# Kernel optimization log

Measured on AMD Instinct MI355X. Metric: run time of the kernel, lower is better.

The kernel has to match this reference:

```python
import jax, jax.numpy as jnp
import numpy as np

E, H, I, T = 8, 1024, 2816, 8192  # experts, hidden, intermediate, total tokens


def setup_inputs() -> dict:
    key = jax.random.key(0)
    k1, k2, k3, k4 = jax.random.split(key, 4)
    x = jax.random.normal(k1, (T, H), dtype=jnp.float32)
    # xavier_normal std = sqrt(2 / (fan_in + fan_out))
    std = (2.0 / (H + I)) ** 0.5
    gate = jax.random.normal(k2, (E, H, I), dtype=jnp.float32) * std
    up = jax.random.normal(k3, (E, H, I), dtype=jnp.float32) * std
    down = jax.random.normal(k4, (E, I, H), dtype=jnp.float32) * std
    # tokens are pre-permuted so each expert's tokens are contiguous; equal split here
    tokens_per_expert = jnp.full((E,), T // E, dtype=jnp.int32)
    return {
        "permuted_local_hidden_states": x,
        "grouped_gate_proj": gate,
        "grouped_up_proj": up,
        "grouped_down_proj": down,
        "tokens_per_expert": tokens_per_expert,
    }


def reference(permuted_local_hidden_states, grouped_gate_proj, grouped_up_proj,
              grouped_down_proj, tokens_per_expert):
    # grouped GEMM: for expert e, rows in its contiguous segment are multiplied by W[e]
    o1 = jax.lax.ragged_dot(permuted_local_hidden_states, grouped_gate_proj,
                            tokens_per_expert)            # [T, I]
    o2 = jax.lax.ragged_dot(permuted_local_hidden_states, grouped_up_proj,
                            tokens_per_expert)            # [T, I]
    inter = jax.nn.silu(o1) * o2                          # SwiGLU  [T, I]
    out = jax.lax.ragged_dot(inter, grouped_down_proj, tokens_per_expert)  # [T, H]
    return out
```

## Files before the change

kernel.cpp:

```cpp
#include <hip/hip_runtime.h>
#include <hip/hip_bf16.h>


#define E_ 8
#define H_ 1024
#define I_ 2816
#define T_ 8192

typedef unsigned short u16;
typedef __attribute__((ext_vector_type(8))) short s16x8;
typedef __attribute__((ext_vector_type(8))) unsigned short u16x8;
typedef __attribute__((ext_vector_type(4))) float f32x4;

__device__ __forceinline__ void async16(const u16* g, u16* l) {
  __builtin_amdgcn_global_load_lds((__attribute__((address_space(1))) void*)g,
                                   (__attribute__((address_space(3))) void*)l, 16, 0, 0);
}

__device__ __forceinline__ u16 f2b(float f) {
  union { __hip_bfloat16 h; u16 u; } c;
  c.h = __float2bfloat16(f);
  return c.u;
}

__global__ __launch_bounds__(256) void convx_k(const float* __restrict__ x,
                                               u16* __restrict__ xb) {
  size_t i = ((size_t)blockIdx.x * 256 + threadIdx.x) * 8;
  float4 v0 = *(const float4*)(x + i);
  float4 v1 = *(const float4*)(x + i + 4);
  u16x8 b;
  b[0] = f2b(v0.x); b[1] = f2b(v0.y); b[2] = f2b(v0.z); b[3] = f2b(v0.w);
  b[4] = f2b(v1.x); b[5] = f2b(v1.y); b[6] = f2b(v1.z); b[7] = f2b(v1.w);
  *(u16x8*)(xb + i) = b;
}

template <int R, int C>
__device__ __forceinline__ void tconv_tile(const float* __restrict__ in,
                                           u16* __restrict__ out,
                                           int bx, int by, int t) {
  const int c0 = bx * 64, r0 = by * 64;
  const int c = c0 + (t >> 2);
  const int rq = (t & 3) * 8;
  const float* p = in + (size_t)r0 * C + c;
  u16* o = out + (size_t)c * R + r0;
  u16x8 b;
#pragma unroll
  for (int j = 0; j < 8; ++j) b[j] = f2b(p[(size_t)(rq + j) * C]);
  *(u16x8*)(o + rq) = b;
#pragma unroll
  for (int j = 0; j < 8; ++j) b[j] = f2b(p[(size_t)(32 + rq + j) * C]);
  *(u16x8*)(o + 32 + rq) = b;
}

__global__ __launch_bounds__(256) void tconvGU_k(const float* __restrict__ G,
                                                 const float* __restrict__ U,
                                                 u16* __restrict__ GT,
                                                 u16* __restrict__ UT) {
  const int z = blockIdx.z;
  const size_t eoff = (size_t)(z >> 1) * (size_t)H_ * I_;
  const float* in = ((z & 1) ? U : G) + eoff;
  u16* out = ((z & 1) ? UT : GT) + eoff;
  tconv_tile<H_, I_>(in, out, blockIdx.x, blockIdx.y, threadIdx.x);
}

__global__ __launch_bounds__(256) void tconvD_k(const float* __restrict__ D,
                                                u16* __restrict__ DT) {
  const size_t eoff = (size_t)blockIdx.z * (size_t)H_ * I_;
  tconv_tile<I_, H_>(D + eoff, DT + eoff, blockIdx.x, blockIdx.y, threadIdx.x);
}

__global__ __launch_bounds__(256, 2) void gemm12_k(
    const u16* __restrict__ X, const u16* __restrict__ GT,
    const u16* __restrict__ UT, const int* __restrict__ tpe,
    u16* __restrict__ inter) {
  __shared__ u16 sA[128 * 64];
  __shared__ u16 sG[64 * 64];
  __shared__ u16 sU[64 * 64];
  const int t = threadIdx.x;
  const int m0 = blockIdx.y * 128;
  const int n0 = blockIdx.x * 64;

  int e = 0, seg_end = T_;
  {
    int s = 0;
    for (int i = 0; i < E_; ++i) {
      int c = tpe[i];
      if (m0 < s + c) { e = i; seg_end = s + c; break; }
      s += c;
    }
  }
  const u16* GTe = GT + (size_t)e * I_ * H_;
  const u16* UTe = UT + (size_t)e * I_ * H_;

  const int sj = ((t & 7) ^ ((t >> 3) & 7)) * 8;
  const u16* gA = X + (size_t)(m0 + (t >> 3)) * H_ + sj;
  const u16* gG = GTe + (size_t)(n0 + (t >> 3)) * H_ + sj;
  const u16* gU = UTe + (size_t)(n0 + (t >> 3)) * H_ + sj;
  u16* lA = sA + t * 8;
  u16* lG = sG + t * 8;
  u16* lU = sU + t * 8;

  const int l = t & 63, w = t >> 6;
  const int wm = (w & 1) * 64, wn = (w >> 1) * 32;
  const int c0 = (((l >> 4) ^ (l & 7))) * 8;
  const u16* fA = sA + (size_t)(wm + (l & 15)) * 64;
  const u16* fG = sG + (size_t)(wn + (l & 15)) * 64;
  const u16* fU = sU + (size_t)(wn + (l & 15)) * 64;

  f32x4 accG[4][2], accU[4][2];
#pragma unroll
  for (int mi = 0; mi < 4; ++mi)
#pragma unroll
    for (int ni = 0; ni < 2; ++ni) {
      accG[mi][ni] = (f32x4){0.f, 0.f, 0.f, 0.f};
      accU[mi][ni] = (f32x4){0.f, 0.f, 0.f, 0.f};
    }

  for (int k0 = 0; k0 < H_; k0 += 64) {
    async16(gA + k0, lA);
    async16(gA + 32 * H_ + k0, lA + 2048);
    async16(gA + 64 * H_ + k0, lA + 4096);
    async16(gA + 96 * H_ + k0, lA + 6144);
    async16(gG + k0, lG);
    async16(gG + 32 * H_ + k0, lG + 2048);
    async16(gU + k0, lU);
    async16(gU + 32 * H_ + k0, lU + 2048);
    __syncthreads();
#pragma unroll
    for (int ks = 0; ks < 2; ++ks) {
      const int co = c0 ^ (ks * 32);
      s16x8 aF[4], gF[2], uF[2];
#pragma unroll
      for (int mi = 0; mi < 4; ++mi) aF[mi] = *(const s16x8*)(fA + mi * 1024 + co);
#pragma unroll
      for (int ni = 0; ni < 2; ++ni) {
        gF[ni] = *(const s16x8*)(fG + ni * 1024 + co);
        uF[ni] = *(const s16x8*)(fU + ni * 1024 + co);
      }
#pragma unroll
      for (int mi = 0; mi < 4; ++mi)
#pragma unroll
        for (int ni = 0; ni < 2; ++ni) {
          accG[mi][ni] = __builtin_amdgcn_mfma_f32_16x16x32_bf16(aF[mi], gF[ni], accG[mi][ni], 0, 0, 0);
          accU[mi][ni] = __builtin_amdgcn_mfma_f32_16x16x32_bf16(aF[mi], uF[ni], accU[mi][ni], 0, 0, 0);
        }
    }
    __syncthreads();
  }

  const int colb = l & 15, rowb = (l >> 4) * 4;
#pragma unroll
  for (int mi = 0; mi < 4; ++mi)
#pragma unroll
    for (int ni = 0; ni < 2; ++ni) {
      const size_t gcol = (size_t)(n0 + wn + ni * 16 + colb);
#pragma unroll
      for (int r = 0; r < 4; ++r) {
        int grow = m0 + wm + mi * 16 + rowb + r;
        if (grow < seg_end) {
          float o1 = accG[mi][ni][r];
          float o2 = accU[mi][ni][r];
          float sv = o1 / (1.f + __expf(-o1));
          inter[(size_t)grow * I_ + gcol] = f2b(sv * o2);
        }
      }
    }
}

__global__ __launch_bounds__(256, 2) void gemm3_k(
    const u16* __restrict__ A, const u16* __restrict__ DT,
    const int* __restrict__ tpe, float* __restrict__ out) {
  __shared__ u16 sA[128 * 64];
  __shared__ u16 sB[64 * 64];
  const int t = threadIdx.x;
  const int m0 = blockIdx.y * 128;
  const int n0 = blockIdx.x * 64;

  int e = 0, seg_end = T_;
  {
    int s = 0;
    for (int i = 0; i < E_; ++i) {
      int c = tpe[i];
      if (m0 < s + c) { e = i; seg_end = s + c; break; }
      s += c;
    }
  }
  const u16* DTe = DT + (size_t)e * H_ * I_;

  const int sj = ((t & 7) ^ ((t >> 3) & 7)) * 8;
  const u16* gA = A + (size_t)(m0 + (t >> 3)) * I_ + sj;
  const u16* gB = DTe + (size_t)(n0 + (t >> 3)) * I_ + sj;
  u16* lA = sA + t * 8;
  u16* lB = sB + t * 8;

  const int l = t & 63, w = t >> 6;
  const int wm = (w & 1) * 64, wn = (w >> 1) * 32;
  const int c0 = (((l >> 4) ^ (l & 7))) * 8;
  const u16* fA = sA + (size_t)(wm + (l & 15)) * 64;
  const u16* fB = sB + (size_t)(wn + (l & 15)) * 64;

  f32x4 acc[4][2];
#pragma unroll
  for (int mi = 0; mi < 4; ++mi)
#pragma unroll
    for (int ni = 0; ni < 2; ++ni) acc[mi][ni] = (f32x4){0.f, 0.f, 0.f, 0.f};

  for (int k0 = 0; k0 < I_; k0 += 64) {
    async16(gA + k0, lA);
    async16(gA + 32 * I_ + k0, lA + 2048);
    async16(gA + 64 * I_ + k0, lA + 4096);
    async16(gA + 96 * I_ + k0, lA + 6144);
    async16(gB + k0, lB);
    async16(gB + 32 * I_ + k0, lB + 2048);
    __syncthreads();
#pragma unroll
    for (int ks = 0; ks < 2; ++ks) {
      const int co = c0 ^ (ks * 32);
      s16x8 aF[4], bF[2];
#pragma unroll
      for (int mi = 0; mi < 4; ++mi) aF[mi] = *(const s16x8*)(fA + mi * 1024 + co);
#pragma unroll
      for (int ni = 0; ni < 2; ++ni) bF[ni] = *(const s16x8*)(fB + ni * 1024 + co);
#pragma unroll
      for (int mi = 0; mi < 4; ++mi)
#pragma unroll
        for (int ni = 0; ni < 2; ++ni)
          acc[mi][ni] = __builtin_amdgcn_mfma_f32_16x16x32_bf16(aF[mi], bF[ni], acc[mi][ni], 0, 0, 0);
    }
    __syncthreads();
  }

  const int colb = l & 15, rowb = (l >> 4) * 4;
#pragma unroll
  for (int mi = 0; mi < 4; ++mi)
#pragma unroll
    for (int ni = 0; ni < 2; ++ni) {
      const size_t gcol = (size_t)(n0 + wn + ni * 16 + colb);
#pragma unroll
      for (int r = 0; r < 4; ++r) {
        int grow = m0 + wm + mi * 16 + rowb + r;
        if (grow < seg_end) out[(size_t)grow * H_ + gcol] = acc[mi][ni][r];
      }
    }
}

extern "C" void kernel_launch(void* const* d_in, const int* in_sizes, int n_in,
                              void* d_out, int out_size, void* d_ws, size_t ws_size,
                              hipStream_t stream) {
  const float* X = (const float*)d_in[0];
  const float* G = (const float*)d_in[1];
  const float* U = (const float*)d_in[2];
  const float* D = (const float*)d_in[3];
  const int* tpe = (const int*)d_in[4];
  float* out = (float*)d_out;

  const size_t W = (size_t)E_ * H_ * I_;
  if (ws_size < 3 * W * sizeof(u16)) return;
  u16* r0 = (u16*)d_ws;
  u16* r1 = r0 + W;
  u16* r2 = r1 + W;
  u16* xb = (u16*)d_out;

  convx_k<<<dim3((T_ * H_) / (256 * 8)), 256, 0, stream>>>(X, xb);
  tconvGU_k<<<dim3(I_ / 64, H_ / 64, E_ * 2), 256, 0, stream>>>(G, U, r0, r1);
  gemm12_k<<<dim3(I_ / 64, T_ / 128), 256, 0, stream>>>(xb, r0, r1, tpe, r2);
  tconvD_k<<<dim3(H_ / 64, I_ / 64, E_), 256, 0, stream>>>(D, r0);
  gemm3_k<<<dim3(H_ / 64, T_ / 128), 256, 0, stream>>>(r2, r0, tpe, out);
}
```

Baseline: 483.7 us.

## Transpose weights through swizzled LDS and widen down-proj GEMM tile to 128x128

The weight transpose-convert kernels now read rows with coalesced float4 loads, write packed bf16 into an XOR-swizzled shared tile, and emit 16-element contiguous stores. The old version did strided scalar reads. Separately, the down-projection GEMM tile grows from 128x64 to 128x128 with a 4x4 MFMA accumulator array per wave. This halves the number of blocks and raises reuse of the A operand, at the cost of more registers and LDS per block and fewer blocks in flight.

```diff
diff --git a/kernel.cpp b/kernel.cpp
--- a/kernel.cpp
+++ b/kernel.cpp
@@ -38,18 +38,36 @@
 __device__ __forceinline__ void tconv_tile(const float* __restrict__ in,
                                            u16* __restrict__ out,
                                            int bx, int by, int t) {
+  __shared__ u16 lt[64 * 64];
   const int c0 = bx * 64, r0 = by * 64;
-  const int c = c0 + (t >> 2);
-  const int rq = (t & 3) * 8;
-  const float* p = in + (size_t)r0 * C + c;
-  u16* o = out + (size_t)c * R + r0;
-  u16x8 b;
-#pragma unroll
-  for (int j = 0; j < 8; ++j) b[j] = f2b(p[(size_t)(rq + j) * C]);
-  *(u16x8*)(o + rq) = b;
-#pragma unroll
-  for (int j = 0; j < 8; ++j) b[j] = f2b(p[(size_t)(32 + rq + j) * C]);
-  *(u16x8*)(o + 32 + rq) = b;
+
+  const int rl = (t >> 3) * 2;
+  const int cl = (t & 7) * 8;
+  const float* p = in + (size_t)(r0 + rl) * C + (c0 + cl);
+  float4 v0 = *(const float4*)(p);
+  float4 v1 = *(const float4*)(p + 4);
+  float4 v2 = *(const float4*)(p + C);
+  float4 v3 = *(const float4*)(p + C + 4);
+
+  float lo[8] = {v0.x, v0.y, v0.z, v0.w, v1.x, v1.y, v1.z, v1.w};
+  float hi[8] = {v2.x, v2.y, v2.z, v2.w, v3.x, v3.y, v3.z, v3.w};
+  const int chunk = ((rl >> 3) ^ (cl >> 3)) << 3;
+  u16* wp = lt + cl * 64 + chunk + (rl & 7);
+#pragma unroll
+  for (int j = 0; j < 8; ++j) {
+    unsigned pk = (unsigned)f2b(lo[j]) | ((unsigned)f2b(hi[j]) << 16);
+    *(unsigned*)(wp + j * 64) = pk;
+  }
+  __syncthreads();
+
+  const int c = t >> 2;
+  const int rs = (t & 3) * 16;
+  const int rc = rs >> 3;
+  u16x8 o0 = *(const u16x8*)(lt + c * 64 + ((rc ^ (c >> 3)) << 3));
+  u16x8 o1 = *(const u16x8*)(lt + c * 64 + (((rc + 1) ^ (c >> 3)) << 3));
+  u16* op = out + (size_t)(c0 + c) * R + (r0 + rs);
+  *(u16x8*)(op) = o0;
+  *(u16x8*)(op + 8) = o1;
 }
 
 __global__ __launch_bounds__(256) void tconvGU_k(const float* __restrict__ G,
@@ -171,10 +189,10 @@
     const u16* __restrict__ A, const u16* __restrict__ DT,
     const int* __restrict__ tpe, float* __restrict__ out) {
   __shared__ u16 sA[128 * 64];
-  __shared__ u16 sB[64 * 64];
+  __shared__ u16 sB[128 * 64];
   const int t = threadIdx.x;
   const int m0 = blockIdx.y * 128;
-  const int n0 = blockIdx.x * 64;
+  const int n0 = blockIdx.x * 128;
 
   int e = 0, seg_end = T_;
   {
@@ -194,16 +212,16 @@
   u16* lB = sB + t * 8;
 
   const int l = t & 63, w = t >> 6;
-  const int wm = (w & 1) * 64, wn = (w >> 1) * 32;
+  const int wm = (w & 1) * 64, wn = (w >> 1) * 64;
   const int c0 = (((l >> 4) ^ (l & 7))) * 8;
   const u16* fA = sA + (size_t)(wm + (l & 15)) * 64;
   const u16* fB = sB + (size_t)(wn + (l & 15)) * 64;
 
-  f32x4 acc[4][2];
-#pragma unroll
-  for (int mi = 0; mi < 4; ++mi)
-#pragma unroll
-    for (int ni = 0; ni < 2; ++ni) acc[mi][ni] = (f32x4){0.f, 0.f, 0.f, 0.f};
+  f32x4 acc[4][4];
+#pragma unroll
+  for (int mi = 0; mi < 4; ++mi)
+#pragma unroll
+    for (int ni = 0; ni < 4; ++ni) acc[mi][ni] = (f32x4){0.f, 0.f, 0.f, 0.f};
 
   for (int k0 = 0; k0 < I_; k0 += 64) {
     async16(gA + k0, lA);
@@ -212,19 +230,21 @@
     async16(gA + 96 * I_ + k0, lA + 6144);
     async16(gB + k0, lB);
     async16(gB + 32 * I_ + k0, lB + 2048);
+    async16(gB + 64 * I_ + k0, lB + 4096);
+    async16(gB + 96 * I_ + k0, lB + 6144);
     __syncthreads();
 #pragma unroll
     for (int ks = 0; ks < 2; ++ks) {
       const int co = c0 ^ (ks * 32);
-      s16x8 aF[4], bF[2];
+      s16x8 aF[4], bF[4];
 #pragma unroll
       for (int mi = 0; mi < 4; ++mi) aF[mi] = *(const s16x8*)(fA + mi * 1024 + co);
 #pragma unroll
-      for (int ni = 0; ni < 2; ++ni) bF[ni] = *(const s16x8*)(fB + ni * 1024 + co);
+      for (int ni = 0; ni < 4; ++ni) bF[ni] = *(const s16x8*)(fB + ni * 1024 + co);
 #pragma unroll
       for (int mi = 0; mi < 4; ++mi)
 #pragma unroll
-        for (int ni = 0; ni < 2; ++ni)
+        for (int ni = 0; ni < 4; ++ni)
           acc[mi][ni] = __builtin_amdgcn_mfma_f32_16x16x32_bf16(aF[mi], bF[ni], acc[mi][ni], 0, 0, 0);
     }
     __syncthreads();
@@ -234,7 +254,7 @@
 #pragma unroll
   for (int mi = 0; mi < 4; ++mi)
 #pragma unroll
-    for (int ni = 0; ni < 2; ++ni) {
+    for (int ni = 0; ni < 4; ++ni) {
       const size_t gcol = (size_t)(n0 + wn + ni * 16 + colb);
 #pragma unroll
       for (int r = 0; r < 4; ++r) {
@@ -265,5 +285,5 @@
   tconvGU_k<<<dim3(I_ / 64, H_ / 64, E_ * 2), 256, 0, stream>>>(G, U, r0, r1);
   gemm12_k<<<dim3(I_ / 64, T_ / 128), 256, 0, stream>>>(xb, r0, r1, tpe, r2);
   tconvD_k<<<dim3(H_ / 64, I_ / 64, E_), 256, 0, stream>>>(D, r0);
-  gemm3_k<<<dim3(H_ / 64, T_ / 128), 256, 0, stream>>>(r2, r0, tpe, out);
-}
+  gemm3_k<<<dim3(H_ / 128, T_ / 128), 256, 0, stream>>>(r2, r0, tpe, out);
+}
```

Result: faster. 464.0 us (-4.1%).
